# Optimization experiments

Hardware: AMD Instinct MI355X
Metric: run time of the kernel (lower is better)

Reference implementation:

```python
import jax, jax.numpy as jnp
import numpy as np

L, S, N, E, H = 2048, 2048, 4, 1024, 16
D = E // H  # head_dim = 64


def setup_inputs() -> dict:
    key = jax.random.key(0)
    ks = jax.random.split(key, 7)
    scale = 1.0 / np.sqrt(E)
    return {
        "query": jax.random.normal(ks[0], (L, N, E), jnp.float32),
        "key": jax.random.normal(ks[1], (S, N, E), jnp.float32),
        "value": jax.random.normal(ks[2], (S, N, E), jnp.float32),
        "in_proj_w": jax.random.normal(ks[3], (3 * E, E), jnp.float32) * scale,
        "in_proj_b": jax.random.normal(ks[4], (3 * E,), jnp.float32) * 0.01,
        "out_proj_w": jax.random.normal(ks[5], (E, E), jnp.float32) * scale * 0.25,
        "out_proj_b": jax.random.normal(ks[6], (E,), jnp.float32) * 0.01,
    }


def reference(query, key, value, in_proj_w, in_proj_b, out_proj_w, out_proj_b):
    # Split packed in-projection into q/k/v parts (torch layout: [3E, E]).
    wq, wk, wv = in_proj_w[:E], in_proj_w[E:2 * E], in_proj_w[2 * E:]
    bq, bk, bv = in_proj_b[:E], in_proj_b[E:2 * E], in_proj_b[2 * E:]

    def proj(x, w, b):  # (T,N,E) -> (N,H,T,D)
        y = jnp.einsum('tne,fe->tnf', x, w) + b
        T = x.shape[0]
        return y.reshape(T, N, H, D).transpose(1, 2, 0, 3)

    q = proj(query, wq, bq) * (1.0 / np.sqrt(D))  # scale queries
    k = proj(key, wk, bk)
    v = proj(value, wv, bv)

    scores = jnp.einsum('nhld,nhsd->nhls', q, k)  # (N,H,L,S)
    attn = jax.nn.softmax(scores, axis=-1)
    ctx = jnp.einsum('nhls,nhsd->nhld', attn, v)  # (N,H,L,D)
    ctx = ctx.transpose(2, 0, 1, 3).reshape(L, N, E)  # (L,N,E)

    out = jnp.einsum('lne,fe->lnf', ctx, out_proj_w) + out_proj_b
    attn_weights = attn.mean(axis=1)  # (N,L,S), averaged over heads (torch default)
    return out, attn_weights
```

## Files before the change

### kernel.cpp

```cpp
#include <hip/hip_runtime.h>
#include <hip/hip_bf16.h>

#define L_ 2048
#define S_ 2048
#define NB 4
#define E_ 1024
#define H_ 16
#define D_ 64
#define LDT 72

typedef __attribute__((ext_vector_type(8))) short bf16x8;
typedef __attribute__((ext_vector_type(4))) float f32x4;

__device__ __forceinline__ short f2bf(float f) {
  union { float f; unsigned u; } v; v.f = f;
  unsigned r = v.u + 0x7FFFu + ((v.u >> 16) & 1u);
  return (short)(r >> 16);
}
__device__ __forceinline__ float bf2f(short s) {
  union { unsigned u; float f; } v; v.u = ((unsigned)(unsigned short)s) << 16;
  return v.f;
}

#define LGKM_BARRIER() do {                                   \
    asm volatile("s_waitcnt lgkmcnt(0)" ::: "memory");        \
    __builtin_amdgcn_sched_barrier(0);                        \
    __builtin_amdgcn_s_barrier();                             \
    __builtin_amdgcn_sched_barrier(0);                        \
  } while (0)

__global__ void k_convert(const float* __restrict__ wi, const float* __restrict__ wo,
                          short* __restrict__ wqkv, short* __restrict__ wout) {
  const int n1 = 3 * E_ * E_ / 4;
  const int n2 = E_ * E_ / 4;
  const int stride = gridDim.x * blockDim.x;
  for (int i = blockIdx.x * blockDim.x + threadIdx.x; i < n1 + n2; i += stride) {
    const float4* s; short* d; int j;
    if (i < n1) { s = (const float4*)wi; d = wqkv; j = i; }
    else        { s = (const float4*)wo; d = wout; j = i - n1; }
    float4 v = s[j];
    short4 o = make_short4(f2bf(v.x), f2bf(v.y), f2bf(v.z), f2bf(v.w));
    *(short4*)&d[(size_t)j * 4] = o;
  }
}

__global__ __launch_bounds__(256) void k_qkv(
    const float* __restrict__ qin, const float* __restrict__ kin, const float* __restrict__ vin,
    const short* __restrict__ wbf, const float* __restrict__ bias,
    short* __restrict__ qh, short* __restrict__ kh, short* __restrict__ vh) {
  __shared__ short As[128 * LDT];
  __shared__ short Bs[128 * LDT];
  const int bm = blockIdx.x;
  const int fbase = blockIdx.y * 128;
  const int mat = fbase >> 10;
  const float* __restrict__ A = (mat == 0) ? qin : (mat == 1) ? kin : vin;
  short* __restrict__ dst = (mat == 0) ? qh : (mat == 1) ? kh : vh;
  const float scale = (mat == 0) ? 0.125f * 1.44269504088896f : 1.0f;
  const int tid = threadIdx.x;
  const int lane = tid & 63, wid = tid >> 6;
  const int wr = wid >> 1, wc = wid & 1;
  const int lr = lane & 15, lk = lane >> 4;
  f32x4 acc[4][4] = {};

  for (int kb = 0; kb < E_; kb += 64) {
#pragma unroll
    for (int i = 0; i < 8; ++i) {
      int f4 = i * 256 + tid;
      int row = f4 >> 4, k4 = f4 & 15;
      float4 v = *(const float4*)&A[(size_t)(bm * 128 + row) * E_ + kb + k4 * 4];
      short4 o = make_short4(f2bf(v.x), f2bf(v.y), f2bf(v.z), f2bf(v.w));
      *(short4*)&As[row * LDT + k4 * 4] = o;
    }
#pragma unroll
    for (int i = 0; i < 4; ++i) {
      int e8 = i * 256 + tid;
      int row = e8 >> 3, k8 = e8 & 7;
      int4 v = *(const int4*)&wbf[(size_t)(fbase + row) * E_ + kb + k8 * 8];
      *(int4*)&Bs[row * LDT + k8 * 8] = v;
    }
    __syncthreads();
#pragma unroll
    for (int kk = 0; kk < 2; ++kk) {
      bf16x8 a[4], b[4];
#pragma unroll
      for (int fi = 0; fi < 4; ++fi)
        a[fi] = *(const bf16x8*)&As[(wr * 64 + fi * 16 + lr) * LDT + kk * 32 + lk * 8];
#pragma unroll
      for (int ci = 0; ci < 4; ++ci)
        b[ci] = *(const bf16x8*)&Bs[(wc * 64 + ci * 16 + lr) * LDT + kk * 32 + lk * 8];
#pragma unroll
      for (int fi = 0; fi < 4; ++fi)
#pragma unroll
        for (int ci = 0; ci < 4; ++ci)
          acc[fi][ci] = __builtin_amdgcn_mfma_f32_16x16x32_bf16(a[fi], b[ci], acc[fi][ci], 0, 0, 0);
    }
    __syncthreads();
  }
#pragma unroll
  for (int ci = 0; ci < 4; ++ci) {
    const int fg = fbase + wc * 64 + ci * 16 + lr;
    const float b = bias[fg];
    const int col = fg & 1023;
    const int h = col >> 6, d = col & 63;
#pragma unroll
    for (int fi = 0; fi < 4; ++fi)
#pragma unroll
      for (int j = 0; j < 4; ++j) {
        int m = bm * 128 + wr * 64 + fi * 16 + lk * 4 + j;
        int t = m >> 2, n = m & 3;
        float vv = (acc[fi][ci][j] + b) * scale;
        dst[(((size_t)(n * H_ + h) * L_ + t) << 6) + d] = f2bf(vv);
      }
  }
}

__global__ __launch_bounds__(256) void k_vtrans(const short* __restrict__ vh,
                                                short* __restrict__ vt) {
  __shared__ short t[64][LDT];
  const int nh = blockIdx.y;
  const int tb = blockIdx.x;
  const int tid = threadIdx.x;
  const short* __restrict__ src = vh + ((size_t)nh * L_ + tb * 64) * D_;
  short* __restrict__ dst = vt + (size_t)nh * S_ * D_;
#pragma unroll
  for (int i = 0; i < 2; ++i) {
    int v = i * 256 + tid;
    int r = v >> 3, c8 = v & 7;
    *(bf16x8*)&t[r][c8 * 8] = *(const bf16x8*)&src[(size_t)r * D_ + c8 * 8];
  }
  __syncthreads();
#pragma unroll
  for (int i = 0; i < 2; ++i) {
    int v = i * 256 + tid;
    int d = v >> 3, t8 = v & 7;
    bf16x8 o;
#pragma unroll
    for (int e = 0; e < 8; ++e) o[e] = t[t8 * 8 + e][d];
    int sb = tb * 2 + (t8 >> 2);
    *(bf16x8*)&dst[(size_t)sb * (D_ * 32) + d * 32 + (t8 & 3) * 8] = o;
  }
}

__global__ __launch_bounds__(256) void k_stats(
    const short* __restrict__ qh, const short* __restrict__ kh, float* __restrict__ rl) {
  const int nh = blockIdx.y;
  const int qt = blockIdx.x;
  const short* __restrict__ Q = qh + (size_t)nh * L_ * D_;
  const short* __restrict__ K = kh + (size_t)nh * S_ * D_;
  const int tid = threadIdx.x;
  const int lane = tid & 63, wid = tid >> 6;
  const int lr = lane & 15, lk = lane >> 4;
  const int rbase = qt * 128 + wid * 32;
  bf16x8 a[2][2];
#pragma unroll
  for (int ri = 0; ri < 2; ++ri)
#pragma unroll
    for (int kk = 0; kk < 2; ++kk)
      a[ri][kk] = *(const bf16x8*)&Q[(size_t)(rbase + ri * 16 + lr) * D_ + kk * 32 + lk * 8];
  float ssum[2][4] = {};
  for (int st = 0; st < S_; st += 64) {
    f32x4 acc[2][4] = {};
#pragma unroll
    for (int ci = 0; ci < 4; ++ci) {
      bf16x8 b0 = *(const bf16x8*)&K[(size_t)(st + ci * 16 + lr) * D_ + lk * 8];
      bf16x8 b1 = *(const bf16x8*)&K[(size_t)(st + ci * 16 + lr) * D_ + 32 + lk * 8];
#pragma unroll
      for (int ri = 0; ri < 2; ++ri) {
        acc[ri][ci] = __builtin_amdgcn_mfma_f32_16x16x32_bf16(a[ri][0], b0, acc[ri][ci], 0, 0, 0);
        acc[ri][ci] = __builtin_amdgcn_mfma_f32_16x16x32_bf16(a[ri][1], b1, acc[ri][ci], 0, 0, 0);
      }
    }
#pragma unroll
    for (int ri = 0; ri < 2; ++ri)
#pragma unroll
      for (int j = 0; j < 4; ++j) {
        float s = __builtin_amdgcn_exp2f(acc[ri][0][j]) + __builtin_amdgcn_exp2f(acc[ri][1][j]) +
                  __builtin_amdgcn_exp2f(acc[ri][2][j]) + __builtin_amdgcn_exp2f(acc[ri][3][j]);
        s += __shfl_xor(s, 1);
        s += __shfl_xor(s, 2);
        s += __shfl_xor(s, 4);
        s += __shfl_xor(s, 8);
        ssum[ri][j] += s;
      }
  }
  if (lr == 0) {
#pragma unroll
    for (int ri = 0; ri < 2; ++ri)
#pragma unroll
      for (int j = 0; j < 4; ++j)
        rl[(size_t)nh * L_ + rbase + ri * 16 + lk * 4 + j] = 1.0f / ssum[ri][j];
  }
}

__global__ __launch_bounds__(512) void k_attn(
    const short* __restrict__ qh, const short* __restrict__ kh, const short* __restrict__ vt,
    const float* __restrict__ rl, float* __restrict__ attnw, short* __restrict__ ctx) {
  __shared__ short psl[16][32][64];
  const int n = blockIdx.y, qt = blockIdx.x;
  const int tid = threadIdx.x;
  const int wid = tid >> 6, lane = tid & 63;
  const int lr = lane & 15, lk = lane >> 4;
  const int rbase = qt * 32;

  const size_t nh0 = (size_t)(n * H_ + wid * 2);
  const short* __restrict__ Kp[2] = { kh + nh0 * S_ * D_, kh + (nh0 + 1) * S_ * D_ };
  const short* __restrict__ Vp[2] = { vt + nh0 * S_ * D_, vt + (nh0 + 1) * S_ * D_ };
  char* slab[2] = { (char*)&psl[wid * 2][0][0], (char*)&psl[wid * 2 + 1][0][0] };

  bf16x8 qf[2][2][2];
  float rls[2][2];
  f32x4 cacc[2][2][4] = {};
#pragma unroll
  for (int hp = 0; hp < 2; ++hp) {
    const short* Q = qh + (nh0 + hp) * L_ * D_;
#pragma unroll
    for (int li = 0; li < 2; ++li) {
#pragma unroll
      for (int kk = 0; kk < 2; ++kk)
        qf[hp][li][kk] = *(const bf16x8*)&Q[(size_t)(rbase + li * 16 + lr) * D_ + kk * 32 + lk * 8];
      rls[hp][li] = rl[(nh0 + hp) * L_ + rbase + li * 16 + lr];
    }
  }
  const int mrow = tid >> 4, mc4 = (tid & 15) * 4;
  float* awp = attnw + ((size_t)n * L_ + rbase + mrow) * S_ + mc4;
  const int mswz = (mc4 * 2) ^ ((mrow & 7) << 4);

  for (int st = 0; st < S_; st += 64) {
#pragma unroll
    for (int hp = 0; hp < 2; ++hp) {
      const short* __restrict__ K = Kp[hp];
      const short* __restrict__ VT = Vp[hp];
      bf16x8 kf[4][2], vb[4][2];
#pragma unroll
      for (int u = 0; u < 4; ++u)
#pragma unroll
        for (int kk = 0; kk < 2; ++kk)
          kf[u][kk] = *(const bf16x8*)&K[(size_t)(st + u * 16 + lr) * D_ + kk * 32 + lk * 8];
#pragma unroll
      for (int b = 0; b < 2; ++b) {
        const size_t sb = (size_t)((st >> 5) + b) * (D_ * 32);
#pragma unroll
        for (int ci = 0; ci < 4; ++ci)
          vb[ci][b] = *(const bf16x8*)&VT[sb + (ci * 16 + lr) * 32 + lk * 8];
      }
      f32x4 sacc[4][2] = {};
#pragma unroll
      for (int u = 0; u < 4; ++u)
#pragma unroll
        for (int li = 0; li < 2; ++li) {
          sacc[u][li] = __builtin_amdgcn_mfma_f32_16x16x32_bf16(kf[u][0], qf[hp][li][0], sacc[u][li], 0, 0, 0);
          sacc[u][li] = __builtin_amdgcn_mfma_f32_16x16x32_bf16(kf[u][1], qf[hp][li][1], sacc[u][li], 0, 0, 0);
        }
#pragma unroll
      for (int u = 0; u < 4; ++u)
#pragma unroll
        for (int li = 0; li < 2; ++li) {
          short4 pk;
          pk.x = f2bf(__builtin_amdgcn_exp2f(sacc[u][li][0]) * rls[hp][li]);
          pk.y = f2bf(__builtin_amdgcn_exp2f(sacc[u][li][1]) * rls[hp][li]);
          pk.z = f2bf(__builtin_amdgcn_exp2f(sacc[u][li][2]) * rls[hp][li]);
          pk.w = f2bf(__builtin_amdgcn_exp2f(sacc[u][li][3]) * rls[hp][li]);
          const int row = li * 16 + lr;
          *(short4*)(slab[hp] + row * 128 + ((u * 32 + lk * 8) ^ ((row & 7) << 4))) = pk;
        }
#pragma unroll
      for (int b = 0; b < 2; ++b)
#pragma unroll
        for (int li = 0; li < 2; ++li) {
          const int row = li * 16 + lr;
          bf16x8 pa = *(const bf16x8*)(slab[hp] + row * 128 + ((b * 64 + lk * 16) ^ ((row & 7) << 4)));
#pragma unroll
          for (int ci = 0; ci < 4; ++ci)
            cacc[hp][li][ci] = __builtin_amdgcn_mfma_f32_16x16x32_bf16(pa, vb[ci][b], cacc[hp][li][ci], 0, 0, 0);
        }
    }
    LGKM_BARRIER();
    {
      float s0 = 0.f, s1 = 0.f, s2 = 0.f, s3 = 0.f;
#pragma unroll
      for (int hh = 0; hh < 16; ++hh) {
        short4 m = *(const short4*)((char*)psl + hh * 4096 + mrow * 128 + mswz);
        s0 += bf2f(m.x); s1 += bf2f(m.y); s2 += bf2f(m.z); s3 += bf2f(m.w);
      }
      *(float4*)&awp[st] = make_float4(s0 * 0.0625f, s1 * 0.0625f, s2 * 0.0625f, s3 * 0.0625f);
    }
    LGKM_BARRIER();
  }
#pragma unroll
  for (int hp = 0; hp < 2; ++hp)
#pragma unroll
    for (int li = 0; li < 2; ++li)
#pragma unroll
      for (int ci = 0; ci < 4; ++ci)
#pragma unroll
        for (int j = 0; j < 4; ++j) {
          int row = rbase + li * 16 + lk * 4 + j;
          int d = ci * 16 + lr;
          ctx[((size_t)row * NB + n) * E_ + (wid * 2 + hp) * 64 + d] = f2bf(cacc[hp][li][ci][j]);
        }
}

__global__ __launch_bounds__(256) void k_out(
    const short* __restrict__ ctxb, const short* __restrict__ wbf,
    const float* __restrict__ bias, float* __restrict__ out) {
  __shared__ short As[128 * LDT];
  __shared__ short Bs[128 * LDT];
  const int bm = blockIdx.x, bn = blockIdx.y;
  const int tid = threadIdx.x;
  const int lane = tid & 63, wid = tid >> 6;
  const int wr = wid >> 1, wc = wid & 1;
  const int lr = lane & 15, lk = lane >> 4;
  f32x4 acc[4][4] = {};
  for (int kb = 0; kb < E_; kb += 64) {
#pragma unroll
    for (int i = 0; i < 4; ++i) {
      int e8 = i * 256 + tid;
      int row = e8 >> 3, k8 = e8 & 7;
      int4 va = *(const int4*)&ctxb[(size_t)(bm * 128 + row) * E_ + kb + k8 * 8];
      *(int4*)&As[row * LDT + k8 * 8] = va;
      int4 vb = *(const int4*)&wbf[(size_t)(bn * 128 + row) * E_ + kb + k8 * 8];
      *(int4*)&Bs[row * LDT + k8 * 8] = vb;
    }
    __syncthreads();
#pragma unroll
    for (int kk = 0; kk < 2; ++kk) {
      bf16x8 a[4], b[4];
#pragma unroll
      for (int fi = 0; fi < 4; ++fi)
        a[fi] = *(const bf16x8*)&As[(wr * 64 + fi * 16 + lr) * LDT + kk * 32 + lk * 8];
#pragma unroll
      for (int ci = 0; ci < 4; ++ci)
        b[ci] = *(const bf16x8*)&Bs[(wc * 64 + ci * 16 + lr) * LDT + kk * 32 + lk * 8];
#pragma unroll
      for (int fi = 0; fi < 4; ++fi)
#pragma unroll
        for (int ci = 0; ci < 4; ++ci)
          acc[fi][ci] = __builtin_amdgcn_mfma_f32_16x16x32_bf16(a[fi], b[ci], acc[fi][ci], 0, 0, 0);
    }
    __syncthreads();
  }
#pragma unroll
  for (int ci = 0; ci < 4; ++ci) {
    int col = bn * 128 + wc * 64 + ci * 16 + lr;
    float b = bias[col];
#pragma unroll
    for (int fi = 0; fi < 4; ++fi)
#pragma unroll
      for (int j = 0; j < 4; ++j) {
        int m = bm * 128 + wr * 64 + fi * 16 + lk * 4 + j;
        out[(size_t)m * E_ + col] = acc[fi][ci][j] + b;
      }
  }
}

extern "C" void kernel_launch(void* const* d_in, const int* in_sizes, int n_in,
                              void* d_out, int out_size, void* d_ws, size_t ws_size,
                              hipStream_t stream) {
  const float* qin = (const float*)d_in[0];
  const float* kin = (const float*)d_in[1];
  const float* vin = (const float*)d_in[2];
  const float* wi  = (const float*)d_in[3];
  const float* bi  = (const float*)d_in[4];
  const float* wo  = (const float*)d_in[5];
  const float* bo  = (const float*)d_in[6];
  float* out = (float*)d_out;
  float* attnw = out + (size_t)L_ * NB * E_;

  short* wqkv = (short*)d_ws;
  short* wout = wqkv + (size_t)3 * E_ * E_;
  short* qh = wout + (size_t)E_ * E_;
  short* kh = qh + (size_t)NB * L_ * E_;
  short* vh = kh + (size_t)NB * L_ * E_;
  short* vt = vh + (size_t)NB * L_ * E_;
  float* rl = (float*)(vt + (size_t)NB * L_ * E_);
  short* ctx = (short*)(rl + (size_t)NB * H_ * L_);

  k_convert<<<1024, 256, 0, stream>>>(wi, wo, wqkv, wout);
  k_qkv<<<dim3(64, 24), 256, 0, stream>>>(qin, kin, vin, wqkv, bi, qh, kh, vh);
  k_vtrans<<<dim3(32, 64), 256, 0, stream>>>(vh, vt);
  k_stats<<<dim3(16, 64), 256, 0, stream>>>(qh, kh, rl);
  k_attn<<<dim3(64, 4), 512, 0, stream>>>(qh, kh, vt, rl, attnw, ctx);
  k_out<<<dim3(64, 8), 256, 0, stream>>>(ctx, wout, bo, out);
}
```

Before: 474.5 us.

## Use one wave per head and double-buffer P slab to overlap head-mean

The attention kernel moves from 512 threads with two heads per wave to 1024 threads with one head per wave, which shrinks per-thread register state. The probability slab becomes double-buffered in 128 KB of dynamic shared memory. The head-averaged attention-weight reduction for chunk ch-1 now runs while chunk ch is computed, so each chunk needs one barrier instead of two. The risks are that 128 KB of LDS per block limits residency to one block per CU, and that 1024-thread blocks carry higher barrier cost.

```diff
diff --git a/kernel.cpp b/kernel.cpp
--- a/kernel.cpp
+++ b/kernel.cpp
@@ -192,112 +192,108 @@
   }
 }
 
-__global__ __launch_bounds__(512) void k_attn(
+__global__ __launch_bounds__(1024) void k_attn(
     const short* __restrict__ qh, const short* __restrict__ kh, const short* __restrict__ vt,
     const float* __restrict__ rl, float* __restrict__ attnw, short* __restrict__ ctx) {
-  __shared__ short psl[16][32][64];
+  extern __shared__ char psl[];
   const int n = blockIdx.y, qt = blockIdx.x;
   const int tid = threadIdx.x;
-  const int wid = tid >> 6, lane = tid & 63;
+  const int h = tid >> 6, lane = tid & 63;
   const int lr = lane & 15, lk = lane >> 4;
   const int rbase = qt * 32;
-
-  const size_t nh0 = (size_t)(n * H_ + wid * 2);
-  const short* __restrict__ Kp[2] = { kh + nh0 * S_ * D_, kh + (nh0 + 1) * S_ * D_ };
-  const short* __restrict__ Vp[2] = { vt + nh0 * S_ * D_, vt + (nh0 + 1) * S_ * D_ };
-  char* slab[2] = { (char*)&psl[wid * 2][0][0], (char*)&psl[wid * 2 + 1][0][0] };
-
-  bf16x8 qf[2][2][2];
-  float rls[2][2];
-  f32x4 cacc[2][2][4] = {};
-#pragma unroll
-  for (int hp = 0; hp < 2; ++hp) {
-    const short* Q = qh + (nh0 + hp) * L_ * D_;
+  const size_t nh = (size_t)(n * H_ + h);
+  const short* __restrict__ K = kh + nh * S_ * D_;
+  const short* __restrict__ VT = vt + nh * S_ * D_;
+  char* const slab0 = psl + h * 4096;
+
+  bf16x8 qf[2][2];
+  float rls[2];
+  {
+    const short* Q = qh + nh * L_ * D_;
 #pragma unroll
     for (int li = 0; li < 2; ++li) {
 #pragma unroll
       for (int kk = 0; kk < 2; ++kk)
-        qf[hp][li][kk] = *(const bf16x8*)&Q[(size_t)(rbase + li * 16 + lr) * D_ + kk * 32 + lk * 8];
-      rls[hp][li] = rl[(nh0 + hp) * L_ + rbase + li * 16 + lr];
-    }
-  }
-  const int mrow = tid >> 4, mc4 = (tid & 15) * 4;
-  float* awp = attnw + ((size_t)n * L_ + rbase + mrow) * S_ + mc4;
-  const int mswz = (mc4 * 2) ^ ((mrow & 7) << 4);
-
-  for (int st = 0; st < S_; st += 64) {
-#pragma unroll
-    for (int hp = 0; hp < 2; ++hp) {
-      const short* __restrict__ K = Kp[hp];
-      const short* __restrict__ VT = Vp[hp];
-      bf16x8 kf[4][2], vb[4][2];
-#pragma unroll
-      for (int u = 0; u < 4; ++u)
-#pragma unroll
-        for (int kk = 0; kk < 2; ++kk)
-          kf[u][kk] = *(const bf16x8*)&K[(size_t)(st + u * 16 + lr) * D_ + kk * 32 + lk * 8];
-#pragma unroll
-      for (int b = 0; b < 2; ++b) {
-        const size_t sb = (size_t)((st >> 5) + b) * (D_ * 32);
+        qf[li][kk] = *(const bf16x8*)&Q[(size_t)(rbase + li * 16 + lr) * D_ + kk * 32 + lk * 8];
+      rls[li] = rl[nh * L_ + rbase + li * 16 + lr];
+    }
+  }
+  f32x4 cacc[2][4] = {};
+  const int mrow = tid >> 5, mc2 = (tid & 31) * 2;
+  float* awp = attnw + ((size_t)n * L_ + rbase + mrow) * S_ + mc2;
+  const int moff = mrow * 128 + ((mc2 * 2) ^ ((mrow & 7) << 4));
+
+  for (int ch = 0; ch < S_ / 64; ++ch) {
+    const int st = ch * 64;
+    char* const sl = slab0 + (ch & 1) * 65536;
+    bf16x8 vb[4][2];
+#pragma unroll
+    for (int b = 0; b < 2; ++b) {
+      const size_t sb = (size_t)((st >> 5) + b) * (D_ * 32);
+#pragma unroll
+      for (int ci = 0; ci < 4; ++ci)
+        vb[ci][b] = *(const bf16x8*)&VT[sb + (ci * 16 + lr) * 32 + lk * 8];
+    }
+#pragma unroll
+    for (int u = 0; u < 4; ++u) {
+      bf16x8 k0 = *(const bf16x8*)&K[(size_t)(st + u * 16 + lr) * D_ + lk * 8];
+      bf16x8 k1 = *(const bf16x8*)&K[(size_t)(st + u * 16 + lr) * D_ + 32 + lk * 8];
+#pragma unroll
+      for (int li = 0; li < 2; ++li) {
+        f32x4 sc = {};
+        sc = __builtin_amdgcn_mfma_f32_16x16x32_bf16(k0, qf[li][0], sc, 0, 0, 0);
+        sc = __builtin_amdgcn_mfma_f32_16x16x32_bf16(k1, qf[li][1], sc, 0, 0, 0);
+        short4 pk;
+        pk.x = f2bf(__builtin_amdgcn_exp2f(sc[0]) * rls[li]);
+        pk.y = f2bf(__builtin_amdgcn_exp2f(sc[1]) * rls[li]);
+        pk.z = f2bf(__builtin_amdgcn_exp2f(sc[2]) * rls[li]);
+        pk.w = f2bf(__builtin_amdgcn_exp2f(sc[3]) * rls[li]);
+        const int row = li * 16 + lr;
+        *(short4*)(sl + row * 128 + ((u * 32 + lk * 8) ^ ((row & 7) << 4))) = pk;
+      }
+    }
+#pragma unroll
+    for (int b = 0; b < 2; ++b)
+#pragma unroll
+      for (int li = 0; li < 2; ++li) {
+        const int row = li * 16 + lr;
+        bf16x8 pa = *(const bf16x8*)(sl + row * 128 + ((b * 64 + lk * 16) ^ ((row & 7) << 4)));
 #pragma unroll
         for (int ci = 0; ci < 4; ++ci)
-          vb[ci][b] = *(const bf16x8*)&VT[sb + (ci * 16 + lr) * 32 + lk * 8];
-      }
-      f32x4 sacc[4][2] = {};
-#pragma unroll
-      for (int u = 0; u < 4; ++u)
-#pragma unroll
-        for (int li = 0; li < 2; ++li) {
-          sacc[u][li] = __builtin_amdgcn_mfma_f32_16x16x32_bf16(kf[u][0], qf[hp][li][0], sacc[u][li], 0, 0, 0);
-          sacc[u][li] = __builtin_amdgcn_mfma_f32_16x16x32_bf16(kf[u][1], qf[hp][li][1], sacc[u][li], 0, 0, 0);
-        }
-#pragma unroll
-      for (int u = 0; u < 4; ++u)
-#pragma unroll
-        for (int li = 0; li < 2; ++li) {
-          short4 pk;
-          pk.x = f2bf(__builtin_amdgcn_exp2f(sacc[u][li][0]) * rls[hp][li]);
-          pk.y = f2bf(__builtin_amdgcn_exp2f(sacc[u][li][1]) * rls[hp][li]);
-          pk.z = f2bf(__builtin_amdgcn_exp2f(sacc[u][li][2]) * rls[hp][li]);
-          pk.w = f2bf(__builtin_amdgcn_exp2f(sacc[u][li][3]) * rls[hp][li]);
-          const int row = li * 16 + lr;
-          *(short4*)(slab[hp] + row * 128 + ((u * 32 + lk * 8) ^ ((row & 7) << 4))) = pk;
-        }
-#pragma unroll
-      for (int b = 0; b < 2; ++b)
-#pragma unroll
-        for (int li = 0; li < 2; ++li) {
-          const int row = li * 16 + lr;
-          bf16x8 pa = *(const bf16x8*)(slab[hp] + row * 128 + ((b * 64 + lk * 16) ^ ((row & 7) << 4)));
-#pragma unroll
-          for (int ci = 0; ci < 4; ++ci)
-            cacc[hp][li][ci] = __builtin_amdgcn_mfma_f32_16x16x32_bf16(pa, vb[ci][b], cacc[hp][li][ci], 0, 0, 0);
-        }
+          cacc[li][ci] = __builtin_amdgcn_mfma_f32_16x16x32_bf16(pa, vb[ci][b], cacc[li][ci], 0, 0, 0);
+      }
+    if (ch > 0) {
+      char* const ms = psl + ((ch & 1) ^ 1) * 65536;
+      float s0 = 0.f, s1 = 0.f;
+#pragma unroll
+      for (int hh = 0; hh < 16; ++hh) {
+        short2 m = *(const short2*)(ms + hh * 4096 + moff);
+        s0 += bf2f(m.x); s1 += bf2f(m.y);
+      }
+      *(float2*)&awp[st - 64] = make_float2(s0 * 0.0625f, s1 * 0.0625f);
     }
     LGKM_BARRIER();
-    {
-      float s0 = 0.f, s1 = 0.f, s2 = 0.f, s3 = 0.f;
-#pragma unroll
-      for (int hh = 0; hh < 16; ++hh) {
-        short4 m = *(const short4*)((char*)psl + hh * 4096 + mrow * 128 + mswz);
-        s0 += bf2f(m.x); s1 += bf2f(m.y); s2 += bf2f(m.z); s3 += bf2f(m.w);
-      }
-      *(float4*)&awp[st] = make_float4(s0 * 0.0625f, s1 * 0.0625f, s2 * 0.0625f, s3 * 0.0625f);
-    }
-    LGKM_BARRIER();
-  }
-#pragma unroll
-  for (int hp = 0; hp < 2; ++hp)
-#pragma unroll
-    for (int li = 0; li < 2; ++li)
-#pragma unroll
-      for (int ci = 0; ci < 4; ++ci)
-#pragma unroll
-        for (int j = 0; j < 4; ++j) {
-          int row = rbase + li * 16 + lk * 4 + j;
-          int d = ci * 16 + lr;
-          ctx[((size_t)row * NB + n) * E_ + (wid * 2 + hp) * 64 + d] = f2bf(cacc[hp][li][ci][j]);
-        }
+  }
+  {
+    char* const ms = psl + 65536;
+    float s0 = 0.f, s1 = 0.f;
+#pragma unroll
+    for (int hh = 0; hh < 16; ++hh) {
+      short2 m = *(const short2*)(ms + hh * 4096 + moff);
+      s0 += bf2f(m.x); s1 += bf2f(m.y);
+    }
+    *(float2*)&awp[S_ - 64] = make_float2(s0 * 0.0625f, s1 * 0.0625f);
+  }
+#pragma unroll
+  for (int li = 0; li < 2; ++li)
+#pragma unroll
+    for (int ci = 0; ci < 4; ++ci)
+#pragma unroll
+      for (int j = 0; j < 4; ++j) {
+        int row = rbase + li * 16 + lk * 4 + j;
+        int d = ci * 16 + lr;
+        ctx[((size_t)row * NB + n) * E_ + h * 64 + d] = f2bf(cacc[li][ci][j]);
+      }
 }
 
 __global__ __launch_bounds__(256) void k_out(
@@ -379,6 +375,6 @@
   k_qkv<<<dim3(64, 24), 256, 0, stream>>>(qin, kin, vin, wqkv, bi, qh, kh, vh);
   k_vtrans<<<dim3(32, 64), 256, 0, stream>>>(vh, vt);
   k_stats<<<dim3(16, 64), 256, 0, stream>>>(qh, kh, rl);
-  k_attn<<<dim3(64, 4), 512, 0, stream>>>(qh, kh, vt, rl, attnw, ctx);
+  k_attn<<<dim3(64, 4), 1024, 131072, stream>>>(qh, kh, vt, rl, attnw, ctx);
   k_out<<<dim3(64, 8), 256, 0, stream>>>(ctx, wout, bo, out);
 }
```

After: 457.7 us. 3.5% less time.
